# Optimization experiments

Hardware: AMD Instinct MI355X
Metric: run time of the kernel (lower is better)

Reference implementation:

```python
import jax, jax.numpy as jnp
import numpy as np

D_MODEL = 1024
NUM_HEADS = 16
D_K = D_MODEL // NUM_HEADS
B, T = 2, 2048


def setup_inputs() -> dict:
    key = jax.random.key(0)
    ks = jax.random.split(key, 11)
    s = 1.0 / np.sqrt(D_MODEL)
    inp = {
        "q": jax.random.normal(ks[0], (B, T, D_MODEL), jnp.float32),
        "k": jax.random.normal(ks[1], (B, T, D_MODEL), jnp.float32),
        "v": jax.random.normal(ks[2], (B, T, D_MODEL), jnp.float32),
        "mask": jnp.tril(jnp.ones((1, 1, T, T), jnp.int32)),  # causal
        "wq": jax.random.normal(ks[3], (D_MODEL, D_MODEL), jnp.float32) * s,
        "bq": jnp.zeros((D_MODEL,), jnp.float32),
        "wk": jax.random.normal(ks[4], (D_MODEL, D_MODEL), jnp.float32) * s,
        "bk": jnp.zeros((D_MODEL,), jnp.float32),
        "wv": jax.random.normal(ks[5], (D_MODEL, D_MODEL), jnp.float32) * s,
        "bv": jnp.zeros((D_MODEL,), jnp.float32),
        "wo": jax.random.normal(ks[6], (D_MODEL, D_MODEL), jnp.float32) * s,
        "bo": jnp.zeros((D_MODEL,), jnp.float32),
    }
    return inp


def reference(q, k, v, mask, wq, bq, wk, bk, wv, bv, wo, bo):
    Bq, Tq, _ = q.shape
    Tk = k.shape[1]
    # projections, split into heads: (B, H, T, d_k)
    qh = (q @ wq + bq).reshape(Bq, Tq, NUM_HEADS, D_K).transpose(0, 2, 1, 3)
    kh = (k @ wk + bk).reshape(Bq, Tk, NUM_HEADS, D_K).transpose(0, 2, 1, 3)
    vh = (v @ wv + bv).reshape(Bq, Tk, NUM_HEADS, D_K).transpose(0, 2, 1, 3)
    scores = jnp.einsum("bhqd,bhkd->bhqk", qh, kh) / jnp.sqrt(jnp.float32(D_K))
    scores = jnp.where(mask == 0, jnp.float32(-1e9), scores)
    attn = jax.nn.softmax(scores, axis=-1)
    ctx = jnp.einsum("bhqk,bhkd->bhqd", attn, vh)
    ctx = ctx.transpose(0, 2, 1, 3).reshape(Bq, Tq, D_MODEL)
    return ctx @ wo + bo
```

## Files before the change

kernel.cpp:

```cpp
#include <hip/hip_runtime.h>
#include <hip/hip_bf16.h>

#define DM 1024
#define NH 16
#define DK 64
#define TT 2048
#define BATCH 2

typedef __attribute__((ext_vector_type(8))) short bf16x8;
typedef __attribute__((ext_vector_type(4))) float f32x4;
typedef __attribute__((ext_vector_type(4))) unsigned short u16x4;
typedef unsigned short u16;

__device__ inline u16 f2b(float x){ __hip_bfloat16 h = __float2bfloat16(x); return *reinterpret_cast<u16*>(&h); }

__device__ inline void gl_lds16(const u16* g, u16* l) {
  __builtin_amdgcn_global_load_lds(
      (const __attribute__((address_space(1))) unsigned int*)g,
      (__attribute__((address_space(3))) unsigned int*)l, 16, 0, 0);
}

__global__ __launch_bounds__(256) void prep(const float* __restrict__ q, const float* __restrict__ k,
                                            const float* __restrict__ v,
                                            const float* __restrict__ wq, const float* __restrict__ wk,
                                            const float* __restrict__ wv, const float* __restrict__ wo,
                                            u16* __restrict__ qb, u16* __restrict__ kb,
                                            u16* __restrict__ vb, u16* __restrict__ wt) {
  int z = blockIdx.z;
  if (z < 3) {
    const float* src = z==0 ? q : z==1 ? k : v;
    u16* dst = z==0 ? qb : z==1 ? kb : vb;
    size_t i = ((size_t)blockIdx.x*256 + threadIdx.x)*8;
    f32x4 a = *(const f32x4*)(src+i);
    f32x4 b = *(const f32x4*)(src+i+4);
    union { bf16x8 v8; u16 e[8]; } u;
    #pragma unroll
    for (int j=0;j<4;j++){ u.e[j] = f2b(a[j]); u.e[4+j] = f2b(b[j]); }
    *(bf16x8*)(dst+i) = u.v8;
  } else {
    int bx = blockIdx.x;
    if (bx >= 1024) return;
    __shared__ float tile[32][33];
    const float* src = z==3 ? wq : z==4 ? wk : z==5 ? wv : wo;
    u16* dst = wt + (size_t)(z-3)*DM*DM;
    int bxx = bx & 31, byy = bx >> 5;
    int tx = threadIdx.x & 31, ty = threadIdx.x >> 5;
    int x  = bxx*32 + tx;
    int y0 = byy*32 + ty;
    #pragma unroll
    for (int i=0;i<32;i+=8) tile[ty+i][tx] = src[(size_t)(y0+i)*DM + x];
    __syncthreads();
    int xo = byy*32 + tx;
    int yo = bxx*32 + ty;
    #pragma unroll
    for (int i=0;i<32;i+=8) dst[(size_t)(yo+i)*DM + xo] = f2b(tile[tx][ty+i]);
  }
}

__device__ __forceinline__ void gemm_body(const u16* __restrict__ A, const u16* __restrict__ W,
                                          const float* __restrict__ bias, u16* __restrict__ outv,
                                          int mode, float oscale) {
  __shared__ u16 As[128*32];
  __shared__ u16 Bs[128*32];
  const int tid = threadIdx.x, lane = tid & 63, wid = tid >> 6;
  const int li = lane & 15, quad = lane >> 4;
  const int row0 = blockIdx.x*128, col0 = blockIdx.y*128;
  const int wr = wid & 1, wc = wid >> 1;

  f32x4 acc[4][4];
  #pragma unroll
  for (int i=0;i<4;i++)
    #pragma unroll
    for (int j=0;j<4;j++) acc[i][j] = f32x4{0.f,0.f,0.f,0.f};

  const int srow = lane >> 2;
  const int scol = (lane & 3) * 8;

  for (int k0 = 0; k0 < DM; k0 += 32) {
    #pragma unroll
    for (int c = 0; c < 2; c++) {
      int ch = wid*2 + c;
      gl_lds16(A + (size_t)(row0 + ch*16 + srow)*DM + k0 + scol, As + ch*512);
      gl_lds16(W + (size_t)(col0 + ch*16 + srow)*DM + k0 + scol, Bs + ch*512);
    }
    __syncthreads();
    bf16x8 a[4], b[4];
    #pragma unroll
    for (int i=0;i<4;i++) a[i] = *(const bf16x8*)&As[(wr*64 + i*16 + li)*32 + quad*8];
    #pragma unroll
    for (int j=0;j<4;j++) b[j] = *(const bf16x8*)&Bs[(wc*64 + j*16 + li)*32 + quad*8];
    #pragma unroll
    for (int i=0;i<4;i++)
      #pragma unroll
      for (int j=0;j<4;j++)
        acc[i][j] = __builtin_amdgcn_mfma_f32_16x16x32_bf16(a[i], b[j], acc[i][j], 0,0,0);
    __syncthreads();
  }

  #pragma unroll
  for (int j=0;j<4;j++) {
    int col = col0 + wc*64 + j*16 + li;
    float bsv = bias[col];
    #pragma unroll
    for (int i=0;i<4;i++) {
      #pragma unroll
      for (int r=0;r<4;r++) {
        int row = row0 + wr*64 + i*16 + quad*4 + r;
        float v = (acc[i][j][r] + bsv) * oscale;
        int bb = row >> 11, t = row & (TT-1);
        int hh = col >> 6,  d = col & 63;
        size_t idx = (mode == 0)
          ? ((((size_t)(bb*NH + hh)*TT + t) << 6) + d)
          : ((((size_t)(bb*NH + hh)*DK + d)*TT) + t);
        outv[idx] = f2b(v);
      }
    }
  }
}

__global__ __launch_bounds__(256) void gemm_qkv(const u16* __restrict__ qb, const u16* __restrict__ kb,
                                                const u16* __restrict__ vb, const u16* __restrict__ wt,
                                                const float* __restrict__ bq, const float* __restrict__ bk,
                                                const float* __restrict__ bv,
                                                u16* __restrict__ qh, u16* __restrict__ kh,
                                                u16* __restrict__ vhT) {
  int z = blockIdx.z;
  const u16* A = z==0 ? qb : z==1 ? kb : vb;
  const u16* W = wt + (size_t)z*DM*DM;
  const float* bias = z==0 ? bq : z==1 ? bk : bv;
  u16* out = z==0 ? qh : z==1 ? kh : vhT;
  gemm_body(A, W, bias, out, z==2 ? 1 : 0, z==0 ? 0.125f : 1.0f);
}

__global__ __launch_bounds__(256) void gemm_out64(const u16* __restrict__ A, const u16* __restrict__ W,
                                                  const float* __restrict__ bias, float* __restrict__ out) {
  __shared__ u16 As[128*32];
  __shared__ u16 Bs[64*32];
  const int tid = threadIdx.x, lane = tid & 63, wid = tid >> 6;
  const int li = lane & 15, quad = lane >> 4;
  const int row0 = blockIdx.x*128, col0 = blockIdx.y*64;
  const int wr = wid & 1, wc = wid >> 1;

  f32x4 acc[4][2];
  #pragma unroll
  for (int i=0;i<4;i++)
    #pragma unroll
    for (int j=0;j<2;j++) acc[i][j] = f32x4{0.f,0.f,0.f,0.f};

  const int srow = lane >> 2;
  const int scol = (lane & 3) * 8;

  for (int k0 = 0; k0 < DM; k0 += 32) {
    #pragma unroll
    for (int c = 0; c < 2; c++) {
      int ch = wid*2 + c;
      gl_lds16(A + (size_t)(row0 + ch*16 + srow)*DM + k0 + scol, As + ch*512);
    }
    gl_lds16(W + (size_t)(col0 + wid*16 + srow)*DM + k0 + scol, Bs + wid*512);
    __syncthreads();
    bf16x8 a[4], b[2];
    #pragma unroll
    for (int i=0;i<4;i++) a[i] = *(const bf16x8*)&As[(wr*64 + i*16 + li)*32 + quad*8];
    #pragma unroll
    for (int j=0;j<2;j++) b[j] = *(const bf16x8*)&Bs[(wc*32 + j*16 + li)*32 + quad*8];
    #pragma unroll
    for (int i=0;i<4;i++)
      #pragma unroll
      for (int j=0;j<2;j++)
        acc[i][j] = __builtin_amdgcn_mfma_f32_16x16x32_bf16(a[i], b[j], acc[i][j], 0,0,0);
    __syncthreads();
  }

  #pragma unroll
  for (int j=0;j<2;j++) {
    int col = col0 + wc*32 + j*16 + li;
    float bsv = bias[col];
    #pragma unroll
    for (int i=0;i<4;i++) {
      #pragma unroll
      for (int r=0;r<4;r++) {
        int row = row0 + wr*64 + i*16 + quad*4 + r;
        out[(size_t)row*DM + col] = acc[i][j][r] + bsv;
      }
    }
  }
}

__global__ __launch_bounds__(256) void flash(const u16* __restrict__ qh, const u16* __restrict__ kh,
                                             const u16* __restrict__ vhT, u16* __restrict__ ctx) {
  const int bh = blockIdx.x;
  const int pr = blockIdx.y;
  const int b = bh >> 4, h = bh & 15;
  const u16* Q  = qh  + (size_t)bh*TT*DK;
  const u16* K  = kh  + (size_t)bh*TT*DK;
  const u16* Vt = vhT + (size_t)bh*DK*TT;

  const int tid = threadIdx.x, lane = tid & 63, wid = tid >> 6;
  const int li = lane & 15, quad = lane >> 4;

  __shared__ u16 Kl[64][72];
  __shared__ u16 Vl[64][72];
  __shared__ u16 Pb[4][16][72];

  const int sr = tid >> 3;
  const int sc = (tid & 7) * 8;

  bf16x8 kr0 = *(const bf16x8*)&K[(size_t)(sr   )*DK + sc];
  bf16x8 kr1 = *(const bf16x8*)&K[(size_t)(sr+32)*DK + sc];
  bf16x8 vr0 = *(const bf16x8*)&Vt[(size_t)(sr   )*TT + sc];
  bf16x8 vr1 = *(const bf16x8*)&Vt[(size_t)(sr+32)*TT + sc];

  #pragma unroll
  for (int ph = 0; ph < 2; ph++) {
    const int qt = (ph == 0) ? pr : (31 - pr);
    const int nt = qt + 1;
    const int qrow0 = qt*64 + wid*16;

    bf16x8 qf0 = *(const bf16x8*)&Q[(size_t)(qrow0+li)*DK +      quad*8];
    bf16x8 qf1 = *(const bf16x8*)&Q[(size_t)(qrow0+li)*DK + 32 + quad*8];

    f32x4 o[4];
    #pragma unroll
    for (int d=0;d<4;d++) o[d] = f32x4{0.f,0.f,0.f,0.f};
    float lp = 0.f;

    for (int it = 0; it < nt; it++) {
      const int k0 = it*64;
      __syncthreads();
      *(bf16x8*)&Kl[sr   ][sc] = kr0;
      *(bf16x8*)&Kl[sr+32][sc] = kr1;
      *(bf16x8*)&Vl[sr   ][sc] = vr0;
      *(bf16x8*)&Vl[sr+32][sc] = vr1;
      __syncthreads();
      if (it+1 < nt) {
        const int k1 = k0 + 64;
        kr0 = *(const bf16x8*)&K[(size_t)(k1+sr   )*DK + sc];
        kr1 = *(const bf16x8*)&K[(size_t)(k1+sr+32)*DK + sc];
        vr0 = *(const bf16x8*)&Vt[(size_t)(sr   )*TT + k1 + sc];
        vr1 = *(const bf16x8*)&Vt[(size_t)(sr+32)*TT + k1 + sc];
      } else if (ph == 0) {
        kr0 = *(const bf16x8*)&K[(size_t)(sr   )*DK + sc];
        kr1 = *(const bf16x8*)&K[(size_t)(sr+32)*DK + sc];
        vr0 = *(const bf16x8*)&Vt[(size_t)(sr   )*TT + sc];
        vr1 = *(const bf16x8*)&Vt[(size_t)(sr+32)*TT + sc];
      }

      f32x4 s[4];
      #pragma unroll
      for (int c=0;c<4;c++) {
        bf16x8 kf0 = *(const bf16x8*)&Kl[c*16+li][     quad*8];
        bf16x8 kf1 = *(const bf16x8*)&Kl[c*16+li][32 + quad*8];
        f32x4 t = __builtin_amdgcn_mfma_f32_16x16x32_bf16(kf0, qf0, f32x4{0.f,0.f,0.f,0.f}, 0,0,0);
        s[c]    = __builtin_amdgcn_mfma_f32_16x16x32_bf16(kf1, qf1, t, 0,0,0);
      }
      const bool dg = (it == nt-1);
      const int qq = qrow0 + li;
      float p[4][4];
      if (dg) {
        #pragma unroll
        for (int c=0;c<4;c++)
          #pragma unroll
          for (int r=0;r<4;r++){
            int key = k0 + c*16 + quad*4 + r;
            p[c][r] = (key <= qq) ? __expf(s[c][r]) : 0.f;
          }
      } else {
        #pragma unroll
        for (int c=0;c<4;c++)
          #pragma unroll
          for (int r=0;r<4;r++)
            p[c][r] = __expf(s[c][r]);
      }
      #pragma unroll
      for (int c=0;c<4;c++)
        #pragma unroll
        for (int r=0;r<4;r++)
          lp += p[c][r];

      #pragma unroll
      for (int c=0;c<4;c++) {
        u16x4 w;
        #pragma unroll
        for (int r=0;r<4;r++) w[r] = f2b(p[c][r]);
        *(u16x4*)&Pb[wid][li][c*16 + quad*4] = w;
      }
      __builtin_amdgcn_wave_barrier();
      __asm__ __volatile__("s_waitcnt lgkmcnt(0)");
      bf16x8 pf0 = *(const bf16x8*)&Pb[wid][li][     quad*8];
      bf16x8 pf1 = *(const bf16x8*)&Pb[wid][li][32 + quad*8];

      #pragma unroll
      for (int d=0;d<4;d++){
        bf16x8 vf0 = *(const bf16x8*)&Vl[d*16+li][     quad*8];
        bf16x8 vf1 = *(const bf16x8*)&Vl[d*16+li][32 + quad*8];
        o[d] = __builtin_amdgcn_mfma_f32_16x16x32_bf16(vf0, pf0, o[d], 0,0,0);
        o[d] = __builtin_amdgcn_mfma_f32_16x16x32_bf16(vf1, pf1, o[d], 0,0,0);
      }
    }

    lp += __shfl_xor(lp, 16, 64);
    lp += __shfl_xor(lp, 32, 64);
    float rl = 1.0f / lp;

    const int qq = qrow0 + li;
    #pragma unroll
    for (int d=0;d<4;d++){
      u16x4 w;
      #pragma unroll
      for (int r=0;r<4;r++) w[r] = f2b(o[d][r] * rl);
      *(u16x4*)&ctx[(size_t)(b*TT + qq)*DM + h*DK + d*16 + quad*4] = w;
    }
  }
}

extern "C" void kernel_launch(void* const* d_in, const int* in_sizes, int n_in,
                              void* d_out, int out_size, void* d_ws, size_t ws_size,
                              hipStream_t stream) {
  const float* q   = (const float*)d_in[0];
  const float* k   = (const float*)d_in[1];
  const float* v   = (const float*)d_in[2];
  const float* wq  = (const float*)d_in[4];
  const float* bq  = (const float*)d_in[5];
  const float* wk  = (const float*)d_in[6];
  const float* bk  = (const float*)d_in[7];
  const float* wv  = (const float*)d_in[8];
  const float* bv  = (const float*)d_in[9];
  const float* wo  = (const float*)d_in[10];
  const float* bo  = (const float*)d_in[11];
  float* out = (float*)d_out;

  const size_t SZ = (size_t)BATCH*TT*DM;
  u16* wt  = (u16*)d_ws;
  u16* qb  = wt + (size_t)4*DM*DM;
  u16* kb  = qb + SZ;
  u16* vb  = kb + SZ;
  u16* qh  = vb + SZ;
  u16* kh  = qh + SZ;
  u16* vhT = kh + SZ;
  u16* ctx = qb;

  prep<<<dim3(2048, 1, 7), 256, 0, stream>>>(q, k, v, wq, wk, wv, wo, qb, kb, vb, wt);

  gemm_qkv<<<dim3(4096/128, DM/128, 3), 256, 0, stream>>>(qb, kb, vb, wt, bq, bk, bv, qh, kh, vhT);

  flash<<<dim3(BATCH*NH, 16), 256, 0, stream>>>(qh, kh, vhT, ctx);

  gemm_out64<<<dim3(4096/128, DM/64), 256, 0, stream>>>(ctx, wt + (size_t)3*DM*DM, bo, out);
}
```

Baseline: 245.5 us.

## Fuse fp32-to-bf16 activation conversion into QKV GEMM and double K-step per sync

The separate pass that converted q/k/v activations from fp32 to bf16 is removed. The QKV GEMM now loads fp32 activations directly, converts them in registers and writes them to LDS, while weights still use direct global-to-LDS loads. Both GEMMs now process 64 K-elements per barrier pair using two LDS sub-tiles, halving the number of synchronizations. The fused path reads fp32 A tiles redundantly across the 8 column blocks (twice the bytes of bf16) and uses synchronous register loads instead of async LDS loads, which may expose latency.

```diff
diff --git a/kernel.cpp b/kernel.cpp
--- a/kernel.cpp
+++ b/kernel.cpp
@@ -20,48 +20,43 @@
       (__attribute__((address_space(3))) unsigned int*)l, 16, 0, 0);
 }
 
-__global__ __launch_bounds__(256) void prep(const float* __restrict__ q, const float* __restrict__ k,
-                                            const float* __restrict__ v,
-                                            const float* __restrict__ wq, const float* __restrict__ wk,
-                                            const float* __restrict__ wv, const float* __restrict__ wo,
-                                            u16* __restrict__ qb, u16* __restrict__ kb,
-                                            u16* __restrict__ vb, u16* __restrict__ wt) {
+__global__ __launch_bounds__(256) void prepw(const float* __restrict__ wq, const float* __restrict__ wk,
+                                             const float* __restrict__ wv, const float* __restrict__ wo,
+                                             u16* __restrict__ wt) {
   int z = blockIdx.z;
-  if (z < 3) {
-    const float* src = z==0 ? q : z==1 ? k : v;
-    u16* dst = z==0 ? qb : z==1 ? kb : vb;
-    size_t i = ((size_t)blockIdx.x*256 + threadIdx.x)*8;
-    f32x4 a = *(const f32x4*)(src+i);
-    f32x4 b = *(const f32x4*)(src+i+4);
-    union { bf16x8 v8; u16 e[8]; } u;
-    #pragma unroll
-    for (int j=0;j<4;j++){ u.e[j] = f2b(a[j]); u.e[4+j] = f2b(b[j]); }
-    *(bf16x8*)(dst+i) = u.v8;
-  } else {
-    int bx = blockIdx.x;
-    if (bx >= 1024) return;
-    __shared__ float tile[32][33];
-    const float* src = z==3 ? wq : z==4 ? wk : z==5 ? wv : wo;
-    u16* dst = wt + (size_t)(z-3)*DM*DM;
-    int bxx = bx & 31, byy = bx >> 5;
-    int tx = threadIdx.x & 31, ty = threadIdx.x >> 5;
-    int x  = bxx*32 + tx;
-    int y0 = byy*32 + ty;
-    #pragma unroll
-    for (int i=0;i<32;i+=8) tile[ty+i][tx] = src[(size_t)(y0+i)*DM + x];
-    __syncthreads();
-    int xo = byy*32 + tx;
-    int yo = bxx*32 + ty;
-    #pragma unroll
-    for (int i=0;i<32;i+=8) dst[(size_t)(yo+i)*DM + xo] = f2b(tile[tx][ty+i]);
-  }
-}
-
-__device__ __forceinline__ void gemm_body(const u16* __restrict__ A, const u16* __restrict__ W,
-                                          const float* __restrict__ bias, u16* __restrict__ outv,
-                                          int mode, float oscale) {
-  __shared__ u16 As[128*32];
-  __shared__ u16 Bs[128*32];
+  __shared__ float tile[32][33];
+  const float* src = z==0 ? wq : z==1 ? wk : z==2 ? wv : wo;
+  u16* dst = wt + (size_t)z*DM*DM;
+  int bx = blockIdx.x;
+  int bxx = bx & 31, byy = bx >> 5;
+  int tx = threadIdx.x & 31, ty = threadIdx.x >> 5;
+  int x  = bxx*32 + tx;
+  int y0 = byy*32 + ty;
+  #pragma unroll
+  for (int i=0;i<32;i+=8) tile[ty+i][tx] = src[(size_t)(y0+i)*DM + x];
+  __syncthreads();
+  int xo = byy*32 + tx;
+  int yo = bxx*32 + ty;
+  #pragma unroll
+  for (int i=0;i<32;i+=8) dst[(size_t)(yo+i)*DM + xo] = f2b(tile[tx][ty+i]);
+}
+
+__global__ __launch_bounds__(256) void gemm_qkv(const float* __restrict__ q, const float* __restrict__ k,
+                                                const float* __restrict__ v, const u16* __restrict__ wt,
+                                                const float* __restrict__ bq, const float* __restrict__ bk,
+                                                const float* __restrict__ bv,
+                                                u16* __restrict__ qh, u16* __restrict__ kh,
+                                                u16* __restrict__ vhT) {
+  const int z = blockIdx.z;
+  const float* A = z==0 ? q : z==1 ? k : v;
+  const u16* W = wt + (size_t)z*DM*DM;
+  const float* bias = z==0 ? bq : z==1 ? bk : bv;
+  u16* outv = z==0 ? qh : z==1 ? kh : vhT;
+  const int mode = (z==2) ? 1 : 0;
+  const float oscale = (z==0) ? 0.125f : 1.0f;
+
+  __shared__ u16 As[2][128*32];
+  __shared__ u16 Bs[2][128*32];
   const int tid = threadIdx.x, lane = tid & 63, wid = tid >> 6;
   const int li = lane & 15, quad = lane >> 4;
   const int row0 = blockIdx.x*128, col0 = blockIdx.y*128;
@@ -76,25 +71,42 @@
   const int srow = lane >> 2;
   const int scol = (lane & 3) * 8;
 
-  for (int k0 = 0; k0 < DM; k0 += 32) {
-    #pragma unroll
-    for (int c = 0; c < 2; c++) {
-      int ch = wid*2 + c;
-      gl_lds16(A + (size_t)(row0 + ch*16 + srow)*DM + k0 + scol, As + ch*512);
-      gl_lds16(W + (size_t)(col0 + ch*16 + srow)*DM + k0 + scol, Bs + ch*512);
-    }
+  for (int k0 = 0; k0 < DM; k0 += 64) {
     __syncthreads();
-    bf16x8 a[4], b[4];
-    #pragma unroll
-    for (int i=0;i<4;i++) a[i] = *(const bf16x8*)&As[(wr*64 + i*16 + li)*32 + quad*8];
-    #pragma unroll
-    for (int j=0;j<4;j++) b[j] = *(const bf16x8*)&Bs[(wc*64 + j*16 + li)*32 + quad*8];
-    #pragma unroll
-    for (int i=0;i<4;i++)
-      #pragma unroll
-      for (int j=0;j<4;j++)
-        acc[i][j] = __builtin_amdgcn_mfma_f32_16x16x32_bf16(a[i], b[j], acc[i][j], 0,0,0);
+    #pragma unroll
+    for (int s=0;s<2;s++)
+      #pragma unroll
+      for (int c=0;c<2;c++) {
+        int ch = wid*2 + c;
+        gl_lds16(W + (size_t)(col0 + ch*16 + srow)*DM + k0 + s*32 + scol, Bs[s] + ch*512);
+      }
+    #pragma unroll
+    for (int s=0;s<2;s++)
+      #pragma unroll
+      for (int c=0;c<2;c++) {
+        int ch = wid*2 + c;
+        const float* ap = A + (size_t)(row0 + ch*16 + srow)*DM + k0 + s*32 + scol;
+        f32x4 lo = *(const f32x4*)ap;
+        f32x4 hi = *(const f32x4*)(ap + 4);
+        union { bf16x8 v8; u16 e[8]; } u;
+        #pragma unroll
+        for (int j=0;j<4;j++){ u.e[j] = f2b(lo[j]); u.e[4+j] = f2b(hi[j]); }
+        *(bf16x8*)&As[s][ch*512 + srow*32 + scol] = u.v8;
+      }
     __syncthreads();
+    #pragma unroll
+    for (int s=0;s<2;s++) {
+      bf16x8 a[4], b[4];
+      #pragma unroll
+      for (int i=0;i<4;i++) a[i] = *(const bf16x8*)&As[s][(wr*64 + i*16 + li)*32 + quad*8];
+      #pragma unroll
+      for (int j=0;j<4;j++) b[j] = *(const bf16x8*)&Bs[s][(wc*64 + j*16 + li)*32 + quad*8];
+      #pragma unroll
+      for (int i=0;i<4;i++)
+        #pragma unroll
+        for (int j=0;j<4;j++)
+          acc[i][j] = __builtin_amdgcn_mfma_f32_16x16x32_bf16(a[i], b[j], acc[i][j], 0,0,0);
+    }
   }
 
   #pragma unroll
@@ -106,36 +118,22 @@
       #pragma unroll
       for (int r=0;r<4;r++) {
         int row = row0 + wr*64 + i*16 + quad*4 + r;
-        float v = (acc[i][j][r] + bsv) * oscale;
+        float vv = (acc[i][j][r] + bsv) * oscale;
         int bb = row >> 11, t = row & (TT-1);
         int hh = col >> 6,  d = col & 63;
         size_t idx = (mode == 0)
           ? ((((size_t)(bb*NH + hh)*TT + t) << 6) + d)
           : ((((size_t)(bb*NH + hh)*DK + d)*TT) + t);
-        outv[idx] = f2b(v);
-      }
-    }
-  }
-}
-
-__global__ __launch_bounds__(256) void gemm_qkv(const u16* __restrict__ qb, const u16* __restrict__ kb,
-                                                const u16* __restrict__ vb, const u16* __restrict__ wt,
-                                                const float* __restrict__ bq, const float* __restrict__ bk,
-                                                const float* __restrict__ bv,
-                                                u16* __restrict__ qh, u16* __restrict__ kh,
-                                                u16* __restrict__ vhT) {
-  int z = blockIdx.z;
-  const u16* A = z==0 ? qb : z==1 ? kb : vb;
-  const u16* W = wt + (size_t)z*DM*DM;
-  const float* bias = z==0 ? bq : z==1 ? bk : bv;
-  u16* out = z==0 ? qh : z==1 ? kh : vhT;
-  gemm_body(A, W, bias, out, z==2 ? 1 : 0, z==0 ? 0.125f : 1.0f);
+        outv[idx] = f2b(vv);
+      }
+    }
+  }
 }
 
 __global__ __launch_bounds__(256) void gemm_out64(const u16* __restrict__ A, const u16* __restrict__ W,
                                                   const float* __restrict__ bias, float* __restrict__ out) {
-  __shared__ u16 As[128*32];
-  __shared__ u16 Bs[64*32];
+  __shared__ u16 As[2][128*32];
+  __shared__ u16 Bs[2][64*32];
   const int tid = threadIdx.x, lane = tid & 63, wid = tid >> 6;
   const int li = lane & 15, quad = lane >> 4;
   const int row0 = blockIdx.x*128, col0 = blockIdx.y*64;
@@ -150,25 +148,31 @@
   const int srow = lane >> 2;
   const int scol = (lane & 3) * 8;
 
-  for (int k0 = 0; k0 < DM; k0 += 32) {
-    #pragma unroll
-    for (int c = 0; c < 2; c++) {
-      int ch = wid*2 + c;
-      gl_lds16(A + (size_t)(row0 + ch*16 + srow)*DM + k0 + scol, As + ch*512);
-    }
-    gl_lds16(W + (size_t)(col0 + wid*16 + srow)*DM + k0 + scol, Bs + wid*512);
+  for (int k0 = 0; k0 < DM; k0 += 64) {
     __syncthreads();
-    bf16x8 a[4], b[2];
-    #pragma unroll
-    for (int i=0;i<4;i++) a[i] = *(const bf16x8*)&As[(wr*64 + i*16 + li)*32 + quad*8];
-    #pragma unroll
-    for (int j=0;j<2;j++) b[j] = *(const bf16x8*)&Bs[(wc*32 + j*16 + li)*32 + quad*8];
-    #pragma unroll
-    for (int i=0;i<4;i++)
-      #pragma unroll
-      for (int j=0;j<2;j++)
-        acc[i][j] = __builtin_amdgcn_mfma_f32_16x16x32_bf16(a[i], b[j], acc[i][j], 0,0,0);
+    #pragma unroll
+    for (int s=0;s<2;s++) {
+      #pragma unroll
+      for (int c=0;c<2;c++) {
+        int ch = wid*2 + c;
+        gl_lds16(A + (size_t)(row0 + ch*16 + srow)*DM + k0 + s*32 + scol, As[s] + ch*512);
+      }
+      gl_lds16(W + (size_t)(col0 + wid*16 + srow)*DM + k0 + s*32 + scol, Bs[s] + wid*512);
+    }
     __syncthreads();
+    #pragma unroll
+    for (int s=0;s<2;s++) {
+      bf16x8 a[4], b[2];
+      #pragma unroll
+      for (int i=0;i<4;i++) a[i] = *(const bf16x8*)&As[s][(wr*64 + i*16 + li)*32 + quad*8];
+      #pragma unroll
+      for (int j=0;j<2;j++) b[j] = *(const bf16x8*)&Bs[s][(wc*32 + j*16 + li)*32 + quad*8];
+      #pragma unroll
+      for (int i=0;i<4;i++)
+        #pragma unroll
+        for (int j=0;j<2;j++)
+          acc[i][j] = __builtin_amdgcn_mfma_f32_16x16x32_bf16(a[i], b[j], acc[i][j], 0,0,0);
+    }
   }
 
   #pragma unroll
@@ -331,17 +335,14 @@
 
   const size_t SZ = (size_t)BATCH*TT*DM;
   u16* wt  = (u16*)d_ws;
-  u16* qb  = wt + (size_t)4*DM*DM;
-  u16* kb  = qb + SZ;
-  u16* vb  = kb + SZ;
-  u16* qh  = vb + SZ;
+  u16* qh  = wt + (size_t)4*DM*DM;
   u16* kh  = qh + SZ;
   u16* vhT = kh + SZ;
-  u16* ctx = qb;
-
-  prep<<<dim3(2048, 1, 7), 256, 0, stream>>>(q, k, v, wq, wk, wv, wo, qb, kb, vb, wt);
-
-  gemm_qkv<<<dim3(4096/128, DM/128, 3), 256, 0, stream>>>(qb, kb, vb, wt, bq, bk, bv, qh, kh, vhT);
+  u16* ctx = vhT + SZ;
+
+  prepw<<<dim3(1024, 1, 4), 256, 0, stream>>>(wq, wk, wv, wo, wt);
+
+  gemm_qkv<<<dim3(4096/128, DM/128, 3), 256, 0, stream>>>(q, k, v, wt, bq, bk, bv, qh, kh, vhT);
 
   flash<<<dim3(BATCH*NH, 16), 256, 0, stream>>>(qh, kh, vhT, ctx);
 
```

Measured after the change: 242.6 us. About the same (-1.2%).
